# Kernel optimization log

Hardware: AMD Instinct MI355X
Metric: run time of the kernel (lower is better)

## Reference

```python
import jax, jax.numpy as jnp
import numpy as np

B, C, H, W = 4, 64, 64, 64
CQK = C // 8


def setup_inputs() -> dict:
    key = jax.random.key(0)
    ks = jax.random.split(key, 4)
    x = jax.random.normal(ks[0], (B, C, H, W), dtype=jnp.float32)
    Wq = jax.random.normal(ks[1], (CQK, C), dtype=jnp.float32) * (1.0 / np.sqrt(C))
    bq = jnp.zeros((CQK,), dtype=jnp.float32)
    Wk = jax.random.normal(ks[2], (CQK, C), dtype=jnp.float32) * (1.0 / np.sqrt(C))
    bk = jnp.zeros((CQK,), dtype=jnp.float32)
    Wv = jax.random.normal(ks[3], (C, C), dtype=jnp.float32) * (1.0 / np.sqrt(C))
    bv = jnp.zeros((C,), dtype=jnp.float32)
    gamma = jnp.ones((1,), dtype=jnp.float32)
    return {"x": x, "Wq": Wq, "bq": bq, "Wk": Wk, "bk": bk,
            "Wv": Wv, "bv": bv, "gamma": gamma}


def reference(x, Wq, bq, Wk, bk, Wv, bv, gamma):
    b, c, h, w = x.shape
    n = h * w
    xf = x.reshape(b, c, n)                      # [B, C, N]
    # 1x1 convs == per-pixel linear over channels
    q = jnp.einsum('oc,bcn->bon', Wq, xf) + bq[:, None]   # [B, C/8, N]
    k = jnp.einsum('oc,bcn->bon', Wk, xf) + bk[:, None]   # [B, C/8, N]
    v = jnp.einsum('oc,bcn->bon', Wv, xf) + bv[:, None]   # [B, C, N]
    # attention_map[b,i,j] = <q[:, i], k[:, j]>; softmax over j
    attn = jax.nn.softmax(jnp.einsum('bci,bcj->bij', q, k), axis=-1)  # [B, N, N]
    # out[b,c,i] = sum_j v[b,c,j] * attn[b,i,j]  (bmm(V, attn^T))
    out = jnp.einsum('bcj,bij->bci', v, attn).reshape(b, c, h, w)
    return gamma * out + x
```

## Files before the change

kernel.cpp:

```cpp
#include <hip/hip_runtime.h>
#include <hip/hip_bf16.h>
#include <math.h>

#define NPIX 4096

typedef __attribute__((ext_vector_type(8))) short s8;
typedef __attribute__((ext_vector_type(4))) float f4;

static __device__ __forceinline__ unsigned packbf2(float a, float b) {
    union { __hip_bfloat162 h; unsigned u; } x;
    x.h = __float22bfloat162_rn(make_float2(a, b));
    return x.u;
}
static __device__ __forceinline__ float2 unpackbf2(unsigned u) {
    float lo = __uint_as_float(u << 16);
    float hi = __uint_as_float(u & 0xffff0000u);
    return make_float2(lo, hi);
}

__global__ __launch_bounds__(512) void prep_kernel(
    const float* __restrict__ x,
    const float* __restrict__ Wq, const float* __restrict__ bq,
    const float* __restrict__ Wk, const float* __restrict__ bk,
    __hip_bfloat16* __restrict__ qbf, __hip_bfloat16* __restrict__ kbf,
    __hip_bfloat16* __restrict__ xbf)
{
    __shared__ float Xp[64][65];
    int t = threadIdx.x;
    int lane = t & 63;
    int grp  = t >> 6;
    int b  = blockIdx.x >> 6;
    int n0 = (blockIdx.x & 63) << 6;

    const float* xb = x + ((size_t)b << 18);
    __hip_bfloat16* xbb = xbf + ((size_t)b << 18);
#pragma unroll
    for (int u = 0; u < 8; ++u) {
        int c = grp + u * 8;
        float v = xb[((size_t)c << 12) + n0 + lane];
        Xp[c][lane] = v;
        xbb[((size_t)c << 12) + n0 + lane] = __float2bfloat16(v);
    }
    __syncthreads();

    float qa = bq[grp], ka = bk[grp];
    const float* wq = Wq + grp * 64;
    const float* wk = Wk + grp * 64;
#pragma unroll
    for (int c = 0; c < 64; ++c) {
        float xv = Xp[c][lane];
        qa = fmaf(wq[c], xv, qa);
        ka = fmaf(wk[c], xv, ka);
    }
    qa *= 1.4426950408889634f;
    int pix = b * NPIX + n0 + lane;
    qbf[(size_t)pix * 8 + grp] = __float2bfloat16(qa);
    kbf[(size_t)pix * 8 + grp] = __float2bfloat16(ka);
}

__global__ __launch_bounds__(256, 4) void flash_part_kernel(
    const __hip_bfloat16* __restrict__ qbf, const __hip_bfloat16* __restrict__ kbf,
    const __hip_bfloat16* __restrict__ xbf,
    __hip_bfloat16* __restrict__ Opart, float* __restrict__ Lp)
{
    __shared__ __align__(16) char pool[34816];
    unsigned short* Xs  = (unsigned short*)pool;
    unsigned short* PTs = (unsigned short*)(pool + 17408);

    int t = threadIdx.x;
    int w    = t >> 6;
    int lane = t & 63;
    int quad = lane >> 4;
    int c16  = lane & 15;

    int blk  = blockIdx.x;
    int sId  = blk >> 8;
    int rest = blk & 255;
    int b    = rest >> 6;
    int i0   = (rest & 63) << 6;
    int jbase = sId << 10;

    const s8 zero8 = {0, 0, 0, 0, 0, 0, 0, 0};
    const f4 zero4 = {0.f, 0.f, 0.f, 0.f};

    s8 qf[4];
#pragma unroll
    for (int it = 0; it < 4; ++it) {
        s8 qv = *(const s8*)(qbf + ((size_t)(b * NPIX + i0 + it * 16 + c16) << 3));
        qf[it] = (quad == 0) ? qv : zero8;
    }

    f4 acc[4];
    float l[4] = {0.f, 0.f, 0.f, 0.f};
#pragma unroll
    for (int ic = 0; ic < 4; ++ic) acc[ic] = zero4;

    const __hip_bfloat16* kb = kbf + ((size_t)(b * NPIX) << 3);
    const unsigned short* xg = (const unsigned short*)xbf + ((size_t)b << 18);

    for (int tile = 0; tile < 8; ++tile) {
        int j0 = jbase + (tile << 7);

        __syncthreads();
        {
            int c = t >> 2, seg = t & 3;
            const uint4* src = (const uint4*)(xg + ((size_t)c << 12) + j0 + seg * 32);
            uint4* dst = (uint4*)(Xs + c * 136 + seg * 32);
#pragma unroll
            for (int u = 0; u < 4; ++u) dst[u] = src[u];
        }
        s8 kf0 = *(const s8*)(kb + ((size_t)(j0 + w * 32 + c16) << 3));
        s8 kf1 = *(const s8*)(kb + ((size_t)(j0 + w * 32 + 16 + c16) << 3));
        __syncthreads();

#pragma unroll
        for (int it = 0; it < 4; ++it) {
            f4 s0 = __builtin_amdgcn_mfma_f32_16x16x32_bf16(kf0, qf[it], zero4, 0, 0, 0);
            f4 s1 = __builtin_amdgcn_mfma_f32_16x16x32_bf16(kf1, qf[it], zero4, 0, 0, 0);
            float e00 = exp2f(s0[0]), e01 = exp2f(s0[1]);
            float e02 = exp2f(s0[2]), e03 = exp2f(s0[3]);
            float e10 = exp2f(s1[0]), e11 = exp2f(s1[1]);
            float e12 = exp2f(s1[2]), e13 = exp2f(s1[3]);
            l[it] += ((e00 + e01) + (e02 + e03)) + ((e10 + e11) + (e12 + e13));
            int i = it * 16 + c16;
            uint2 pk0, pk1;
            pk0.x = packbf2(e00, e01); pk0.y = packbf2(e02, e03);
            pk1.x = packbf2(e10, e11); pk1.y = packbf2(e12, e13);
            *(uint2*)(PTs + i * 136 + w * 32 + quad * 4) = pk0;
            *(uint2*)(PTs + i * 136 + w * 32 + 16 + quad * 4) = pk1;
        }
        __syncthreads();

#pragma unroll
        for (int kc = 0; kc < 4; ++kc) {
            s8 xf = *(const s8*)(Xs + (w * 16 + c16) * 136 + kc * 32 + quad * 8);
#pragma unroll
            for (int ic = 0; ic < 4; ++ic) {
                s8 pf = *(const s8*)(PTs + (ic * 16 + c16) * 136 + kc * 32 + quad * 8);
                acc[ic] = __builtin_amdgcn_mfma_f32_16x16x32_bf16(xf, pf, acc[ic], 0, 0, 0);
            }
        }
    }

    float* Osh = (float*)pool;
    float* Lsh = (float*)(pool + 17408);

#pragma unroll
    for (int it = 0; it < 4; ++it) {
        l[it] += __shfl_xor(l[it], 16);
        l[it] += __shfl_xor(l[it], 32);
    }
    __syncthreads();
    if (quad == 0) {
#pragma unroll
        for (int it = 0; it < 4; ++it) Lsh[w * 64 + it * 16 + c16] = l[it];
    }
#pragma unroll
    for (int ic = 0; ic < 4; ++ic) {
        f4 v = acc[ic];
        *(float4*)(Osh + (ic * 16 + c16) * 68 + w * 16 + quad * 4) =
            make_float4(v[0], v[1], v[2], v[3]);
    }
    __syncthreads();

    if (t < 64)
        Lp[(size_t)blk * 64 + t] = Lsh[t] + Lsh[64 + t] + Lsh[128 + t] + Lsh[192 + t];

    {
        int i = t >> 2, c0 = (t & 3) << 4;
        const float* src = Osh + i * 68 + c0;
        uint4 lo, hi;
        lo.x = packbf2(src[0], src[1]);   lo.y = packbf2(src[2], src[3]);
        lo.z = packbf2(src[4], src[5]);   lo.w = packbf2(src[6], src[7]);
        hi.x = packbf2(src[8], src[9]);   hi.y = packbf2(src[10], src[11]);
        hi.z = packbf2(src[12], src[13]); hi.w = packbf2(src[14], src[15]);
        uint4* dst = (uint4*)(Opart + (size_t)blk * 4096 + i * 64 + c0);
        dst[0] = lo; dst[1] = hi;
    }
}

__global__ __launch_bounds__(512) void merge_kernel(
    const __hip_bfloat16* __restrict__ Opart, const float* __restrict__ Lp,
    const float* __restrict__ Wv, const float* __restrict__ bv,
    const float* __restrict__ x, const float* __restrict__ gamma,
    float* __restrict__ out)
{
    __shared__ float Osh[64 * 68];
    __shared__ float Wvs[4096];
    __shared__ float LinvS[64];
    __shared__ float bvs[64];

    int t = threadIdx.x;
    int b  = blockIdx.x >> 6;
    int i0 = (blockIdx.x & 63) << 6;

    if (t < 64) {
        int i = t;
        float lt = Lp[(size_t)(0 * 256 + blockIdx.x) * 64 + i]
                 + Lp[(size_t)(1 * 256 + blockIdx.x) * 64 + i]
                 + Lp[(size_t)(2 * 256 + blockIdx.x) * 64 + i]
                 + Lp[(size_t)(3 * 256 + blockIdx.x) * 64 + i];
        LinvS[i] = 1.0f / lt;
        bvs[i] = bv[i];
    }
    {
        const float4* wsrc = (const float4*)Wv;
        float4* wdst = (float4*)Wvs;
        wdst[t] = wsrc[t];
        wdst[t + 512] = wsrc[t + 512];
    }
    __syncthreads();

    {
        int i = t >> 3, c0 = (t & 7) << 3;
        float o[8];
#pragma unroll
        for (int k = 0; k < 8; ++k) o[k] = 0.f;
#pragma unroll
        for (int sId = 0; sId < 4; ++sId) {
            size_t base = (size_t)(sId * 256 + blockIdx.x) * 4096 + i * 64 + c0;
            uint4 pk = *(const uint4*)(Opart + base);
            float2 e0 = unpackbf2(pk.x), e1 = unpackbf2(pk.y);
            float2 e2 = unpackbf2(pk.z), e3 = unpackbf2(pk.w);
            o[0] += e0.x; o[1] += e0.y; o[2] += e1.x; o[3] += e1.y;
            o[4] += e2.x; o[5] += e2.y; o[6] += e3.x; o[7] += e3.y;
        }
        float* dst = Osh + i * 68 + c0;
        *(float4*)(dst + 0) = make_float4(o[0], o[1], o[2], o[3]);
        *(float4*)(dst + 4) = make_float4(o[4], o[5], o[6], o[7]);
    }
    __syncthreads();

    {
        int i  = t & 63;
        int cg = t >> 6;
        float inv = LinvS[i];
        float res[8];
#pragma unroll
        for (int k = 0; k < 8; ++k) res[k] = 0.f;
#pragma unroll 4
        for (int cb = 0; cb < 16; ++cb) {
            float4 o = *(const float4*)(Osh + i * 68 + cb * 4);
#pragma unroll
            for (int k = 0; k < 8; ++k) {
                float4 wv4 = *(const float4*)(Wvs + (cg * 8 + k) * 64 + cb * 4);
                res[k] = fmaf(wv4.x, o.x, fmaf(wv4.y, o.y, fmaf(wv4.z, o.z, fmaf(wv4.w, o.w, res[k]))));
            }
        }
        float g = gamma[0];
        const float* xr = x + ((size_t)b << 18) + i0;
        float* outp = out + ((size_t)b << 18) + i0;
#pragma unroll
        for (int k = 0; k < 8; ++k) {
            int c = cg * 8 + k;
            float attn = fmaf(res[k], inv, bvs[c]);
            size_t off = ((size_t)c << 12) + i;
            outp[off] = fmaf(g, attn, xr[off]);
        }
    }
}

extern "C" void kernel_launch(void* const* d_in, const int* in_sizes, int n_in,
                              void* d_out, int out_size, void* d_ws, size_t ws_size,
                              hipStream_t stream) {
    const float* x     = (const float*)d_in[0];
    const float* Wq    = (const float*)d_in[1];
    const float* bq    = (const float*)d_in[2];
    const float* Wk    = (const float*)d_in[3];
    const float* bk    = (const float*)d_in[4];
    const float* Wv    = (const float*)d_in[5];
    const float* bv    = (const float*)d_in[6];
    const float* gamma = (const float*)d_in[7];
    float* out = (float*)d_out;

    __hip_bfloat16* qbf   = (__hip_bfloat16*)d_ws;
    __hip_bfloat16* kbf   = qbf + (size_t)4 * NPIX * 8;
    __hip_bfloat16* xbf   = kbf + (size_t)4 * NPIX * 8;
    __hip_bfloat16* Opart = xbf + (size_t)4 * NPIX * 64;
    float* Lp = (float*)(Opart + (size_t)1024 * 4096);

    prep_kernel<<<256, 512, 0, stream>>>(x, Wq, bq, Wk, bk, qbf, kbf, xbf);
    flash_part_kernel<<<1024, 256, 0, stream>>>(qbf, kbf, xbf, Opart, Lp);
    merge_kernel<<<256, 512, 0, stream>>>(Opart, Lp, Wv, bv, x, gamma, out);
}
```

Measured before the change: 115.0 us.

## Use 32x32x16 MFMA for the PV product and drop a redundant barrier

The P·X accumulation now runs one 32x32x16 bf16 MFMA chain per wave over a 32x32 output quadrant instead of four 16x16x32 chains. This cuts the number of MFMA issues and LDS fragment reads per tile. The X tile is loaded into registers and stored to LDS without the barrier that used to sit between the staging and the score computation. That is safe because Xs is only read after the barrier following the PTs writes. The epilogue now scatters 16 scalar floats per lane into shared memory instead of writing float4 vectors, which adds some store cost and possible bank conflicts.

```diff
diff --git a/kernel.cpp b/kernel.cpp
--- a/kernel.cpp
+++ b/kernel.cpp
@@ -6,6 +6,7 @@
 
 typedef __attribute__((ext_vector_type(8))) short s8;
 typedef __attribute__((ext_vector_type(4))) float f4;
+typedef __attribute__((ext_vector_type(16))) float f16v;
 
 static __device__ __forceinline__ unsigned packbf2(float a, float b) {
     union { __hip_bfloat162 h; unsigned u; } x;
@@ -72,6 +73,10 @@
     int lane = t & 63;
     int quad = lane >> 4;
     int c16  = lane & 15;
+    int l32  = lane & 31;
+    int lh   = lane >> 5;
+    int chalf = w & 1;
+    int ihalf = w >> 1;
 
     int blk  = blockIdx.x;
     int sId  = blk >> 8;
@@ -90,10 +95,10 @@
         qf[it] = (quad == 0) ? qv : zero8;
     }
 
-    f4 acc[4];
+    f16v acc = {0.f};
+#pragma unroll
+    for (int r = 0; r < 16; ++r) acc[r] = 0.f;
     float l[4] = {0.f, 0.f, 0.f, 0.f};
-#pragma unroll
-    for (int ic = 0; ic < 4; ++ic) acc[ic] = zero4;
 
     const __hip_bfloat16* kb = kbf + ((size_t)(b * NPIX) << 3);
     const unsigned short* xg = (const unsigned short*)xbf + ((size_t)b << 18);
@@ -102,16 +107,17 @@
         int j0 = jbase + (tile << 7);
 
         __syncthreads();
-        {
-            int c = t >> 2, seg = t & 3;
-            const uint4* src = (const uint4*)(xg + ((size_t)c << 12) + j0 + seg * 32);
-            uint4* dst = (uint4*)(Xs + c * 136 + seg * 32);
-#pragma unroll
-            for (int u = 0; u < 4; ++u) dst[u] = src[u];
-        }
+
+        int c = t >> 2, seg = t & 3;
+        const uint4* src = (const uint4*)(xg + ((size_t)c << 12) + j0 + seg * 32);
+        uint4 sv0 = src[0], sv1 = src[1], sv2 = src[2], sv3 = src[3];
         s8 kf0 = *(const s8*)(kb + ((size_t)(j0 + w * 32 + c16) << 3));
         s8 kf1 = *(const s8*)(kb + ((size_t)(j0 + w * 32 + 16 + c16) << 3));
-        __syncthreads();
+
+        {
+            uint4* dst = (uint4*)(Xs + c * 136 + seg * 32);
+            dst[0] = sv0; dst[1] = sv1; dst[2] = sv2; dst[3] = sv3;
+        }
 
 #pragma unroll
         for (int it = 0; it < 4; ++it) {
@@ -132,13 +138,10 @@
         __syncthreads();
 
 #pragma unroll
-        for (int kc = 0; kc < 4; ++kc) {
-            s8 xf = *(const s8*)(Xs + (w * 16 + c16) * 136 + kc * 32 + quad * 8);
-#pragma unroll
-            for (int ic = 0; ic < 4; ++ic) {
-                s8 pf = *(const s8*)(PTs + (ic * 16 + c16) * 136 + kc * 32 + quad * 8);
-                acc[ic] = __builtin_amdgcn_mfma_f32_16x16x32_bf16(xf, pf, acc[ic], 0, 0, 0);
-            }
+        for (int q = 0; q < 8; ++q) {
+            s8 xf = *(const s8*)(Xs  + (chalf * 32 + l32) * 136 + q * 16 + lh * 8);
+            s8 pf = *(const s8*)(PTs + (ihalf * 32 + l32) * 136 + q * 16 + lh * 8);
+            acc = __builtin_amdgcn_mfma_f32_32x32x16_bf16(xf, pf, acc, 0, 0, 0);
         }
     }
 
@@ -155,11 +158,13 @@
 #pragma unroll
         for (int it = 0; it < 4; ++it) Lsh[w * 64 + it * 16 + c16] = l[it];
     }
-#pragma unroll
-    for (int ic = 0; ic < 4; ++ic) {
-        f4 v = acc[ic];
-        *(float4*)(Osh + (ic * 16 + c16) * 68 + w * 16 + quad * 4) =
-            make_float4(v[0], v[1], v[2], v[3]);
+    {
+        int i = ihalf * 32 + l32;
+#pragma unroll
+        for (int r = 0; r < 16; ++r) {
+            int cc = chalf * 32 + (r & 3) + 8 * (r >> 2) + 4 * lh;
+            Osh[i * 68 + cc] = acc[r];
+        }
     }
     __syncthreads();
 
```

After: 111.0 us. 1.04x faster.
